# Kernel tuning notes

Measured on AMD Instinct MI355X. Metric: run time of the kernel, lower is better.

Reference implementation:

```python
import jax, jax.numpy as jnp
import numpy as np

FEAT_DIM = 128
GUIDE_DIM = 128
NIR_DIM = 32
H_LR, W_LR = 128, 128
H_HR, W_HR = 256, 256
IMNET_IN = FEAT_DIM + 2 * GUIDE_DIM + 2  # 386


def make_coord_1d(n):
    # pixel-center coords in [-1, 1]: (2i+1)/n - 1
    return (2.0 * jnp.arange(n, dtype=jnp.float32) + 1.0) / n - 1.0


def nearest_sample(img, cy, cx):
    """F.grid_sample(img, grid, mode='nearest', align_corners=False, padding='zeros').
    img: [b, C, h, w]; cy, cx: [N] normalized coords (cy -> h axis, cx -> w axis).
    Returns sampled values [b, C, N] and the pixel-center coords (qcy, qcx) the
    nearest sample corresponds to (0 when out of range, matching zero padding)."""
    h, w = img.shape[-2], img.shape[-1]
    iy = jnp.round(((cy + 1.0) * h - 1.0) * 0.5).astype(jnp.int32)  # round-half-even == nearbyint
    ix = jnp.round(((cx + 1.0) * w - 1.0) * 0.5).astype(jnp.int32)
    valid = (iy >= 0) & (iy < h) & (ix >= 0) & (ix < w)
    iyc = jnp.clip(iy, 0, h - 1)
    ixc = jnp.clip(ix, 0, w - 1)
    out = img[:, :, iyc, ixc]                       # [b, C, N] gather
    out = jnp.where(valid[None, None, :], out, 0.0)
    qcy = jnp.where(valid, (2.0 * iyc.astype(jnp.float32) + 1.0) / h - 1.0, 0.0)
    qcx = jnp.where(valid, (2.0 * ixc.astype(jnp.float32) + 1.0) / w - 1.0, 0.0)
    return out, qcy, qcx


def mlp(x, W1, b1, W2, b2, W3, b3):
    x = jax.nn.relu(x @ W1 + b1)
    x = jax.nn.relu(x @ W2 + b2)
    return x @ W3 + b3


def setup_inputs() -> dict:
    key = jax.random.key(0)
    ks = jax.random.split(key, 9)
    return {
        "feat": jax.random.normal(ks[0], (1, FEAT_DIM, H_LR, W_LR), jnp.float32),
        "lr_guide": jax.random.normal(ks[1], (1, GUIDE_DIM, H_LR, W_LR), jnp.float32),
        "hr_guide": jax.random.normal(ks[2], (1, GUIDE_DIM, H_HR, W_HR), jnp.float32),
        "W1": jax.random.normal(ks[3], (IMNET_IN, 256), jnp.float32) * 0.05,
        "b1": jax.random.normal(ks[4], (256,), jnp.float32) * 0.05,
        "W2": jax.random.normal(ks[5], (256, 128), jnp.float32) * 0.05,
        "b2": jax.random.normal(ks[6], (128,), jnp.float32) * 0.05,
        "W3": jax.random.normal(ks[7], (128, NIR_DIM), jnp.float32) * 0.05,
        "b3": jax.random.normal(ks[8], (NIR_DIM,), jnp.float32) * 0.05,
    }


def reference(feat, lr_guide, hr_guide, W1, b1, W2, b2, W3, b3):
    b, _, h, w = feat.shape
    _, cg, H, W = hr_guide.shape
    N = H * W
    featc = jnp.concatenate([lr_guide, feat], axis=1)        # [b, guide+feat, h, w]

    gy, gx = jnp.meshgrid(make_coord_1d(H), make_coord_1d(W), indexing="ij")
    cy = gy.reshape(-1)                                      # [N] coord[:, 0] (h axis)
    cx = gx.reshape(-1)                                      # [N] coord[:, 1] (w axis)

    q_guide_hr = hr_guide.reshape(b, cg, N).transpose(0, 2, 1)  # [b, N, cg]

    # feat_ : gather at the unshifted coord (identical across neighbors)
    feat_b, _, _ = nearest_sample(featc, cy, cx)
    feat_b = feat_b.transpose(0, 2, 1)                       # [b, N, C]

    rx = 1.0 / h
    ry = 1.0 / w
    preds, gcs = [], []
    for vx in (-1.0, 1.0):
        for vy in (-1.0, 1.0):
            q_feat, qcy, qcx = nearest_sample(featc, cy + vx * rx, cx + vy * ry)
            q_feat = q_feat.transpose(0, 2, 1)               # [b, N, C]
            rel = jnp.stack([(cy - qcy) * h, (cx - qcx) * w], axis=-1)  # [N, 2]
            rel = jnp.broadcast_to(rel[None], (b, N, 2))
            inp = jnp.concatenate([q_feat, q_guide_hr, rel], axis=-1)  # [b, N, 386]
            preds.append(mlp(inp, W1, b1, W2, b2, W3, b3))   # [b, N, NIR]
            # bilateral color weight: dot over channels [-4:-1]
            gcs.append(jnp.sum(feat_b[..., -4:-1] * q_feat[..., -4:-1], axis=-1))
    preds = jnp.stack(preds, axis=-1)                        # [b, N, NIR, 4]
    weight = jax.nn.softmax(jnp.stack(gcs, axis=-1), axis=-1)  # [b, N, 4]
    ret = jnp.sum(preds * weight[:, :, None, :], axis=-1)    # [b, N, NIR]
    return ret.transpose(0, 2, 1).reshape(b, -1, H, W)
```

## Files before the change

kernel.cpp:

```cpp
#include <hip/hip_runtime.h>
#include <hip/hip_bf16.h>


using bf16x8 = __attribute__((ext_vector_type(8))) __bf16;
using f32x4  = __attribute__((ext_vector_type(4))) float;

__device__ __forceinline__ float bf2f(unsigned short u){
  unsigned int x = ((unsigned int)u) << 16;
  return __builtin_bit_cast(float, x);
}
__device__ __forceinline__ unsigned short f2bf(float f){
  unsigned int x = __builtin_bit_cast(unsigned int, f);
  unsigned int r = x + 0x7fffu + ((x >> 16) & 1u);
  return (unsigned short)(r >> 16);
}
__device__ __forceinline__ bf16x8 ld8(const ushort* p){
  uint4 r = *(const uint4*)p;
  return __builtin_bit_cast(bf16x8, r);
}

struct RowMeta { int spos; float relY, relX; };
__device__ __forceinline__ RowMeta row_meta(int Y, int X, int br){
  int ivx = br >> 1, ivy = br & 1;
  int validY, iy; float relY;
  if (ivx == 0){ validY = (Y >= 1);   iy = (Y-1) >> 1; relY = (Y & 1) ?  0.5f :  1.5f; }
  else         { validY = (Y <= 254); iy = (Y+1) >> 1; relY = (Y & 1) ? -1.5f : -0.5f; }
  int validX, ix; float relX;
  if (ivy == 0){ validX = (X >= 1);   ix = (X-1) >> 1; relX = (X & 1) ?  0.5f :  1.5f; }
  else         { validX = (X <= 254); ix = (X+1) >> 1; relX = (X & 1) ? -1.5f : -0.5f; }
  RowMeta r;
  if (validY && validX){ r.spos = iy*128 + ix; r.relY = relY; r.relX = relX; }
  else { r.spos = -1; r.relY = (float)Y + 0.5f - 128.0f; r.relX = (float)X + 0.5f - 128.0f; }
  return r;
}

__global__ __launch_bounds__(256) void convert_weights(
    const float* __restrict__ W1, const float* __restrict__ W2,
    const float* __restrict__ W3,
    ushort* __restrict__ W1t,
    ushort* __restrict__ W2t,
    ushort* __restrict__ W3t)
{
  int i = blockIdx.x*256 + threadIdx.x;
  { int k = i >> 8, n = i & 255; W1t[n*384 + k] = f2bf(W1[i]); }
  if (i < 32768){ int k = i >> 7, n = i & 127; W2t[n*256 + k] = f2bf(W2[i]); }
  if (i < 4096) { int k = i >> 5, n = i & 31;  W3t[n*128 + k] = f2bf(W3[i]); }
}

__global__ __launch_bounds__(256) void stage1_gemm(
    const float* __restrict__ src0, const float* __restrict__ src1, int M,
    const ushort* __restrict__ Bt, int koff,
    const float* __restrict__ bias,
    ushort* __restrict__ outp)
{
  __shared__ ushort A[64*136];
  const int t = threadIdx.x;
  const int w = t >> 6, lane = t & 63, quad = lane >> 4, l15 = lane & 15;
  const int pos0 = blockIdx.x * 64;
  const int nhalf = src1 ? 2 : 1;

  f32x4 acc[4][4];
  #pragma unroll
  for (int mt=0; mt<4; mt++)
    #pragma unroll
    for (int nt=0; nt<4; nt++) acc[mt][nt] = f32x4{0.f,0.f,0.f,0.f};

  for (int h=0; h<nhalf; h++){
    const float* src = h ? src1 : src0;
    #pragma unroll
    for (int i=0; i<32; i++){
      int f = i*256 + t;
      int k = f >> 6, mm = f & 63;
      A[mm*136 + k] = f2bf(src[(size_t)k*M + pos0 + mm]);
    }
    __syncthreads();
    bf16x8 b[4][4];
    #pragma unroll
    for (int kt=0; kt<4; kt++)
      #pragma unroll
      for (int nt=0; nt<4; nt++)
        b[kt][nt] = ld8(&Bt[(size_t)(w*64 + nt*16 + l15)*384 + koff + h*128 + kt*32 + quad*8]);
    #pragma unroll
    for (int mt=0; mt<4; mt++)
      #pragma unroll
      for (int kt=0; kt<4; kt++){
        bf16x8 a = ld8(&A[(mt*16 + l15)*136 + kt*32 + quad*8]);
        #pragma unroll
        for (int nt=0; nt<4; nt++)
          acc[mt][nt] = __builtin_amdgcn_mfma_f32_16x16x32_bf16(a, b[kt][nt], acc[mt][nt], 0,0,0);
      }
    __syncthreads();
  }
  #pragma unroll
  for (int mt=0; mt<4; mt++)
    #pragma unroll
    for (int nt=0; nt<4; nt++){
      int n = w*64 + nt*16 + l15;
      float bv = bias ? bias[n] : 0.0f;
      #pragma unroll
      for (int r=0; r<4; r++){
        int mm = mt*16 + quad*4 + r;
        outp[(size_t)(pos0 + mm)*256 + n] = f2bf(acc[mt][nt][r] + bv);
      }
    }
}

__global__ __launch_bounds__(256, 3) void main_fused(
    const float* __restrict__ feat,
    const float* __restrict__ hr_guide,
    const float* __restrict__ W1,
    const float* __restrict__ b1v,
    const float* __restrict__ b2v,
    const float* __restrict__ b3v,
    const ushort* __restrict__ U,
    const ushort* __restrict__ W1t,
    const ushort* __restrict__ W2t,
    const ushort* __restrict__ W3t,
    float* __restrict__ outp)
{
  __shared__ __align__(16) ushort A1[64*264];
  __shared__ __align__(16) ushort Gt[16*264];
  __shared__ __align__(16) float  w1r[2][256];
  __shared__ float gcs[64];
  __shared__ float wgt[64];

  const int t = threadIdx.x;
  const int w = t >> 6, lane = t & 63, quad = lane >> 4, l15 = lane & 15;
  const int Y  = blockIdx.x >> 4;
  const int X0 = (blockIdx.x & 15) << 4;

  const int m   = t >> 2;
  const int pix = m >> 2, br = m & 3;
  const int c0  = (t & 3) * 64;
  RowMeta rm = row_meta(Y, X0 + pix, br);

  uint4 uu[8];
  if (rm.spos >= 0){
    const ushort* Up = U + (size_t)rm.spos*256 + c0;
    #pragma unroll
    for (int j=0; j<8; j++) uu[j] = *(const uint4*)(Up + j*8);
  } else {
    #pragma unroll
    for (int j=0; j<8; j++) uu[j] = make_uint4(0u,0u,0u,0u);
  }

  {
    ushort* Ahr = A1;
    #pragma unroll
    for (int i=0; i<2; i++){
      int id = i*256 + t;
      int ch = id >> 2, xq = id & 3;
      float4 v = *(const float4*)(hr_guide + (size_t)ch*65536 + Y*256 + X0 + xq*4);
      Ahr[(xq*4+0)*136 + ch] = f2bf(v.x);
      Ahr[(xq*4+1)*136 + ch] = f2bf(v.y);
      Ahr[(xq*4+2)*136 + ch] = f2bf(v.z);
      Ahr[(xq*4+3)*136 + ch] = f2bf(v.w);
    }
  }
  w1r[0][t] = W1[384*256 + t];
  w1r[1][t] = W1[385*256 + t];

  if (t < 64){
    RowMeta g = row_meta(Y, X0 + (t>>2), t & 3);
    float gc = 0.0f;
    if (g.spos >= 0){
      int bpos = (Y>>1)*128 + ((X0 + (t>>2)) >> 1);
      #pragma unroll
      for (int cc=0; cc<3; cc++)
        gc += feat[(size_t)(124+cc)*16384 + bpos] * feat[(size_t)(124+cc)*16384 + g.spos];
    }
    gcs[t] = gc;
  }
  __syncthreads();

  if (t < 16){
    float g0 = gcs[t*4+0], g1 = gcs[t*4+1], g2 = gcs[t*4+2], g3 = gcs[t*4+3];
    float mx = fmaxf(fmaxf(g0,g1), fmaxf(g2,g3));
    float e0 = __expf(g0-mx), e1 = __expf(g1-mx), e2 = __expf(g2-mx), e3 = __expf(g3-mx);
    float inv = 1.0f/(e0+e1+e2+e3);
    wgt[t*4+0]=e0*inv; wgt[t*4+1]=e1*inv; wgt[t*4+2]=e2*inv; wgt[t*4+3]=e3*inv;
  }
  {
    f32x4 accg[4];
    #pragma unroll
    for (int nt=0; nt<4; nt++) accg[nt] = f32x4{0.f,0.f,0.f,0.f};
    #pragma unroll
    for (int kt=0; kt<4; kt++){
      bf16x8 a = ld8(&A1[l15*136 + kt*32 + quad*8]);
      #pragma unroll
      for (int nt=0; nt<4; nt++){
        bf16x8 b = ld8(&W1t[(size_t)(w*64 + nt*16 + l15)*384 + 256 + kt*32 + quad*8]);
        accg[nt] = __builtin_amdgcn_mfma_f32_16x16x32_bf16(a, b, accg[nt], 0,0,0);
      }
    }
    #pragma unroll
    for (int nt=0; nt<4; nt++){
      int n = w*64 + nt*16 + l15;
      float bv = b1v[n];
      #pragma unroll
      for (int r=0; r<4; r++)
        Gt[(quad*4+r)*264 + n] = f2bf(accg[nt][r] + bv);
    }
  }
  __syncthreads();

  bf16x8 b2f[8][2];
  #pragma unroll
  for (int kt=0; kt<8; kt++)
    #pragma unroll
    for (int nt=0; nt<2; nt++)
      b2f[kt][nt] = ld8(&W2t[(size_t)(w*32 + nt*16 + l15)*256 + kt*32 + quad*8]);

  {
    float relY = rm.relY, relX = rm.relX;
    #pragma unroll
    for (int jj=0; jj<8; jj++){
      int c = c0 + jj*8;
      union { uint4 v; ushort s[8]; } gu, uv, ov;
      gu.v = *(const uint4*)&Gt[pix*264 + c];
      uv.v = uu[jj];
      float r0[8], r1[8];
      *(float4*)&r0[0] = *(const float4*)&w1r[0][c];
      *(float4*)&r0[4] = *(const float4*)&w1r[0][c+4];
      *(float4*)&r1[0] = *(const float4*)&w1r[1][c];
      *(float4*)&r1[4] = *(const float4*)&w1r[1][c+4];
      #pragma unroll
      for (int i=0; i<8; i++){
        float h = bf2f(uv.s[i]) + bf2f(gu.s[i]) + relY*r0[i] + relX*r1[i];
        ov.s[i] = f2bf(fmaxf(h, 0.0f));
      }
      *(uint4*)&A1[m*264 + c] = ov.v;
    }
  }
  __syncthreads();

  f32x4 acc2[4][2];
  #pragma unroll
  for (int mt=0; mt<4; mt++)
    #pragma unroll
    for (int nt=0; nt<2; nt++) acc2[mt][nt] = f32x4{0.f,0.f,0.f,0.f};
  #pragma unroll
  for (int mt=0; mt<4; mt++)
    #pragma unroll
    for (int kt=0; kt<8; kt++){
      bf16x8 a = ld8(&A1[(mt*16 + l15)*264 + kt*32 + quad*8]);
      #pragma unroll
      for (int nt=0; nt<2; nt++)
        acc2[mt][nt] = __builtin_amdgcn_mfma_f32_16x16x32_bf16(a, b2f[kt][nt], acc2[mt][nt], 0,0,0);
    }
  __syncthreads();

  bf16x8 b3f[4][2];
  #pragma unroll
  for (int kt=0; kt<4; kt++)
    #pragma unroll
    for (int nt=0; nt<2; nt++)
      b3f[kt][nt] = ld8(&W3t[(size_t)(nt*16 + l15)*128 + kt*32 + quad*8]);

  {
    ushort* A2 = A1;
    float bias0 = b2v[w*32 + l15], bias1 = b2v[w*32 + 16 + l15];
    #pragma unroll
    for (int mt=0; mt<4; mt++)
      #pragma unroll
      for (int nt=0; nt<2; nt++){
        int n = w*32 + nt*16 + l15;
        float bv = nt ? bias1 : bias0;
        #pragma unroll
        for (int r=0; r<4; r++){
          int mm = mt*16 + quad*4 + r;
          A2[mm*136 + n] = f2bf(fmaxf(acc2[mt][nt][r] + bv, 0.0f));
        }
      }
  }
  __syncthreads();

  {
    const ushort* A2 = A1;
    f32x4 acc3[2] = { f32x4{0.f,0.f,0.f,0.f}, f32x4{0.f,0.f,0.f,0.f} };
    #pragma unroll
    for (int kt=0; kt<4; kt++){
      bf16x8 a = ld8(&A2[(w*16 + l15)*136 + kt*32 + quad*8]);
      #pragma unroll
      for (int nt=0; nt<2; nt++)
        acc3[nt] = __builtin_amdgcn_mfma_f32_16x16x32_bf16(a, b3f[kt][nt], acc3[nt], 0,0,0);
    }
    int lp = w*4 + quad;
    int X = X0 + lp;
    float w0 = wgt[lp*4+0], w1 = wgt[lp*4+1], w2 = wgt[lp*4+2], w3 = wgt[lp*4+3];
    #pragma unroll
    for (int nt=0; nt<2; nt++){
      int n = nt*16 + l15;
      float bb = b3v[n];
      float v = w0*(acc3[nt][0]+bb) + w1*(acc3[nt][1]+bb)
              + w2*(acc3[nt][2]+bb) + w3*(acc3[nt][3]+bb);
      outp[(size_t)n*65536 + (size_t)Y*256 + X] = v;
    }
  }
}

extern "C" void kernel_launch(void* const* d_in, const int* in_sizes, int n_in,
                              void* d_out, int out_size, void* d_ws, size_t ws_size,
                              hipStream_t stream)
{
  const float* feat     = (const float*)d_in[0];
  const float* lr_guide = (const float*)d_in[1];
  const float* hr_guide = (const float*)d_in[2];
  const float* W1       = (const float*)d_in[3];
  const float* b1       = (const float*)d_in[4];
  const float* W2       = (const float*)d_in[5];
  const float* b2       = (const float*)d_in[6];
  const float* W3       = (const float*)d_in[7];
  const float* b3       = (const float*)d_in[8];
  float* outp = (float*)d_out;

  char* ws = (char*)d_ws;
  ushort* W1t = (ushort*)(ws);
  ushort* W2t = (ushort*)(ws + 196608);
  ushort* W3t = (ushort*)(ws + 196608 + 65536);
  ushort* Ub  = (ushort*)(ws + 196608 + 65536 + 8192);

  convert_weights<<<384, 256, 0, stream>>>(W1, W2, W3, W1t, W2t, W3t);
  stage1_gemm<<<256, 256, 0, stream>>>(lr_guide, feat, 16384, W1t, 0, nullptr, Ub);
  main_fused<<<4096, 256, 0, stream>>>(feat, hr_guide, W1, b1, b2, b3,
                                       Ub, W1t, W2t, W3t, outp);
}
```

Measured before the change: 204.1 us.

## Fold layer-1 gather, rel and bias terms into a single MFMA K-slice

The layer-1 epilogue used to gather precomputed U rows, add the hr-guide GEMM result and apply the rel/bias terms in scalar code. It now appends a fifth MFMA K-step whose A operand holds gathered U entries plus the rel weights and bias rows, and whose B operand is a one-hot selector built per row. That removes the Gt staging buffer, one barrier and the scalar pass, and lets occupancy rise to 4 blocks. The stage-1 GEMM is also split into smaller 32-row, half-N blocks so more of them launch. The cost is scattered 2-byte gathers from Ub and some extra MFMA work.

After: 207.8 us. Within noise of the previous version (+1.8%).

```diff
diff --git a/kernel.cpp b/kernel.cpp
--- a/kernel.cpp
+++ b/kernel.cpp
@@ -19,7 +19,7 @@
   return __builtin_bit_cast(bf16x8, r);
 }
 
-struct RowMeta { int spos; float relY, relX; };
+struct RowMeta { int valid, ix; float relY, relX; int spos; };
 __device__ __forceinline__ RowMeta row_meta(int Y, int X, int br){
   int ivx = br >> 1, ivy = br & 1;
   int validY, iy; float relY;
@@ -29,98 +29,96 @@
   if (ivy == 0){ validX = (X >= 1);   ix = (X-1) >> 1; relX = (X & 1) ?  0.5f :  1.5f; }
   else         { validX = (X <= 254); ix = (X+1) >> 1; relX = (X & 1) ? -1.5f : -0.5f; }
   RowMeta r;
-  if (validY && validX){ r.spos = iy*128 + ix; r.relY = relY; r.relX = relX; }
-  else { r.spos = -1; r.relY = (float)Y + 0.5f - 128.0f; r.relX = (float)X + 0.5f - 128.0f; }
+  r.valid = validY && validX;
+  r.ix = ix;
+  if (r.valid){ r.relY = relY; r.relX = relX; r.spos = iy*128 + ix; }
+  else { r.relY = (float)Y + 0.5f - 128.0f; r.relX = (float)X + 0.5f - 128.0f; r.spos = -1; }
   return r;
 }
 
 __global__ __launch_bounds__(256) void convert_weights(
-    const float* __restrict__ W1, const float* __restrict__ W2,
-    const float* __restrict__ W3,
+    const float* __restrict__ W1, const float* __restrict__ b1,
+    const float* __restrict__ W2, const float* __restrict__ W3,
     ushort* __restrict__ W1t,
     ushort* __restrict__ W2t,
-    ushort* __restrict__ W3t)
+    ushort* __restrict__ W3t,
+    ushort* __restrict__ Ub)
 {
-  int i = blockIdx.x*256 + threadIdx.x;
-  { int k = i >> 8, n = i & 255; W1t[n*384 + k] = f2bf(W1[i]); }
-  if (i < 32768){ int k = i >> 7, n = i & 127; W2t[n*256 + k] = f2bf(W2[i]); }
-  if (i < 4096) { int k = i >> 5, n = i & 31;  W3t[n*128 + k] = f2bf(W3[i]); }
+  int b = blockIdx.x, t = threadIdx.x;
+  if (b < 384){
+    int i = b*256 + t;
+    { int k = i >> 8, n = i & 255; W1t[n*384 + k] = f2bf(W1[i]); }
+    if (i < 32768){ int k = i >> 7, n = i & 127; W2t[n*256 + k] = f2bf(W2[i]); }
+    if (i < 4096) { int k = i >> 5, n = i & 31;  W3t[n*128 + k] = f2bf(W3[i]); }
+  } else {
+    int r = b - 384;
+    float v = (r == 0) ? W1[384*256 + t] : (r == 1) ? W1[385*256 + t]
+            : (r == 2) ? b1[t] : 0.0f;
+    Ub[(size_t)(16384 + r)*256 + t] = f2bf(v);
+  }
 }
 
 __global__ __launch_bounds__(256) void stage1_gemm(
-    const float* __restrict__ src0, const float* __restrict__ src1, int M,
-    const ushort* __restrict__ Bt, int koff,
-    const float* __restrict__ bias,
+    const float* __restrict__ src0, const float* __restrict__ src1,
+    const ushort* __restrict__ W1t,
     ushort* __restrict__ outp)
 {
-  __shared__ ushort A[64*136];
+  __shared__ ushort A[32*136];
   const int t = threadIdx.x;
   const int w = t >> 6, lane = t & 63, quad = lane >> 4, l15 = lane & 15;
-  const int pos0 = blockIdx.x * 64;
-  const int nhalf = src1 ? 2 : 1;
-
-  f32x4 acc[4][4];
-  #pragma unroll
-  for (int mt=0; mt<4; mt++)
-    #pragma unroll
-    for (int nt=0; nt<4; nt++) acc[mt][nt] = f32x4{0.f,0.f,0.f,0.f};
-
-  for (int h=0; h<nhalf; h++){
+  const int pos0  = (blockIdx.x >> 1) * 32;
+  const int nside = (blockIdx.x & 1) * 128;
+  const int mt = w >> 1;
+  const int ntb = (w & 1) * 4;
+
+  f32x4 acc[4];
+  #pragma unroll
+  for (int nt=0; nt<4; nt++) acc[nt] = f32x4{0.f,0.f,0.f,0.f};
+
+  for (int h=0; h<2; h++){
     const float* src = h ? src1 : src0;
     #pragma unroll
-    for (int i=0; i<32; i++){
+    for (int i=0; i<16; i++){
       int f = i*256 + t;
-      int k = f >> 6, mm = f & 63;
-      A[mm*136 + k] = f2bf(src[(size_t)k*M + pos0 + mm]);
+      int k = f >> 5, mm = f & 31;
+      A[mm*136 + k] = f2bf(src[(size_t)k*16384 + pos0 + mm]);
     }
     __syncthreads();
-    bf16x8 b[4][4];
-    #pragma unroll
-    for (int kt=0; kt<4; kt++)
-      #pragma unroll
-      for (int nt=0; nt<4; nt++)
-        b[kt][nt] = ld8(&Bt[(size_t)(w*64 + nt*16 + l15)*384 + koff + h*128 + kt*32 + quad*8]);
-    #pragma unroll
-    for (int mt=0; mt<4; mt++)
-      #pragma unroll
-      for (int kt=0; kt<4; kt++){
-        bf16x8 a = ld8(&A[(mt*16 + l15)*136 + kt*32 + quad*8]);
-        #pragma unroll
-        for (int nt=0; nt<4; nt++)
-          acc[mt][nt] = __builtin_amdgcn_mfma_f32_16x16x32_bf16(a, b[kt][nt], acc[mt][nt], 0,0,0);
+    #pragma unroll
+    for (int kt=0; kt<4; kt++){
+      bf16x8 a = ld8(&A[(mt*16 + l15)*136 + kt*32 + quad*8]);
+      #pragma unroll
+      for (int nt=0; nt<4; nt++){
+        bf16x8 b = ld8(&W1t[(size_t)(nside + (ntb+nt)*16 + l15)*384 + h*128 + kt*32 + quad*8]);
+        acc[nt] = __builtin_amdgcn_mfma_f32_16x16x32_bf16(a, b, acc[nt], 0,0,0);
       }
+    }
     __syncthreads();
   }
   #pragma unroll
-  for (int mt=0; mt<4; mt++)
-    #pragma unroll
-    for (int nt=0; nt<4; nt++){
-      int n = w*64 + nt*16 + l15;
-      float bv = bias ? bias[n] : 0.0f;
-      #pragma unroll
-      for (int r=0; r<4; r++){
-        int mm = mt*16 + quad*4 + r;
-        outp[(size_t)(pos0 + mm)*256 + n] = f2bf(acc[mt][nt][r] + bv);
-      }
-    }
-}
-
-__global__ __launch_bounds__(256, 3) void main_fused(
+  for (int nt=0; nt<4; nt++){
+    int n = nside + (ntb+nt)*16 + l15;
+    #pragma unroll
+    for (int r=0; r<4; r++){
+      int mm = mt*16 + quad*4 + r;
+      outp[(size_t)(pos0 + mm)*256 + n] = f2bf(acc[nt][r]);
+    }
+  }
+}
+
+__global__ __launch_bounds__(256, 4) void main_fused(
     const float* __restrict__ feat,
     const float* __restrict__ hr_guide,
-    const float* __restrict__ W1,
-    const float* __restrict__ b1v,
     const float* __restrict__ b2v,
     const float* __restrict__ b3v,
-    const ushort* __restrict__ U,
+    const ushort* __restrict__ Ub,
     const ushort* __restrict__ W1t,
     const ushort* __restrict__ W2t,
     const ushort* __restrict__ W3t,
     float* __restrict__ outp)
 {
   __shared__ __align__(16) ushort A1[64*264];
-  __shared__ __align__(16) ushort Gt[16*264];
-  __shared__ __align__(16) float  w1r[2][256];
+  __shared__ __align__(16) ushort Ahr[16*136];
   __shared__ float gcs[64];
   __shared__ float wgt[64];
 
@@ -128,38 +126,19 @@
   const int w = t >> 6, lane = t & 63, quad = lane >> 4, l15 = lane & 15;
   const int Y  = blockIdx.x >> 4;
   const int X0 = (blockIdx.x & 15) << 4;
-
-  const int m   = t >> 2;
-  const int pix = m >> 2, br = m & 3;
-  const int c0  = (t & 3) * 64;
-  RowMeta rm = row_meta(Y, X0 + pix, br);
-
-  uint4 uu[8];
-  if (rm.spos >= 0){
-    const ushort* Up = U + (size_t)rm.spos*256 + c0;
-    #pragma unroll
-    for (int j=0; j<8; j++) uu[j] = *(const uint4*)(Up + j*8);
-  } else {
-    #pragma unroll
-    for (int j=0; j<8; j++) uu[j] = make_uint4(0u,0u,0u,0u);
-  }
-
-  {
-    ushort* Ahr = A1;
-    #pragma unroll
-    for (int i=0; i<2; i++){
-      int id = i*256 + t;
-      int ch = id >> 2, xq = id & 3;
-      float4 v = *(const float4*)(hr_guide + (size_t)ch*65536 + Y*256 + X0 + xq*4);
-      Ahr[(xq*4+0)*136 + ch] = f2bf(v.x);
-      Ahr[(xq*4+1)*136 + ch] = f2bf(v.y);
-      Ahr[(xq*4+2)*136 + ch] = f2bf(v.z);
-      Ahr[(xq*4+3)*136 + ch] = f2bf(v.w);
-    }
-  }
-  w1r[0][t] = W1[384*256 + t];
-  w1r[1][t] = W1[385*256 + t];
-
+  const int iyA = (Y-1) >> 1, iyB = (Y+1) >> 1;
+  const int ixbase = (X0-1) >> 1;
+
+  #pragma unroll
+  for (int i=0; i<2; i++){
+    int id = i*256 + t;
+    int ch = id >> 2, xq = id & 3;
+    float4 v = *(const float4*)(hr_guide + (size_t)ch*65536 + Y*256 + X0 + xq*4);
+    Ahr[(xq*4+0)*136 + ch] = f2bf(v.x);
+    Ahr[(xq*4+1)*136 + ch] = f2bf(v.y);
+    Ahr[(xq*4+2)*136 + ch] = f2bf(v.z);
+    Ahr[(xq*4+3)*136 + ch] = f2bf(v.w);
+  }
   if (t < 64){
     RowMeta g = row_meta(Y, X0 + (t>>2), t & 3);
     float gc = 0.0f;
@@ -172,7 +151,6 @@
     gcs[t] = gc;
   }
   __syncthreads();
-
   if (t < 16){
     float g0 = gcs[t*4+0], g1 = gcs[t*4+1], g2 = gcs[t*4+2], g3 = gcs[t*4+3];
     float mx = fmaxf(fmaxf(g0,g1), fmaxf(g2,g3));
@@ -180,26 +158,66 @@
     float inv = 1.0f/(e0+e1+e2+e3);
     wgt[t*4+0]=e0*inv; wgt[t*4+1]=e1*inv; wgt[t*4+2]=e2*inv; wgt[t*4+3]=e3*inv;
   }
-  {
-    f32x4 accg[4];
-    #pragma unroll
-    for (int nt=0; nt<4; nt++) accg[nt] = f32x4{0.f,0.f,0.f,0.f};
-    #pragma unroll
-    for (int kt=0; kt<4; kt++){
-      bf16x8 a = ld8(&A1[l15*136 + kt*32 + quad*8]);
-      #pragma unroll
-      for (int nt=0; nt<4; nt++){
-        bf16x8 b = ld8(&W1t[(size_t)(w*64 + nt*16 + l15)*384 + 256 + kt*32 + quad*8]);
-        accg[nt] = __builtin_amdgcn_mfma_f32_16x16x32_bf16(a, b, accg[nt], 0,0,0);
-      }
-    }
-    #pragma unroll
-    for (int nt=0; nt<4; nt++){
-      int n = w*64 + nt*16 + l15;
-      float bv = b1v[n];
-      #pragma unroll
-      for (int r=0; r<4; r++)
-        Gt[(quad*4+r)*264 + n] = f2bf(accg[nt][r] + bv);
+
+  int uoff[8];
+  #pragma unroll
+  for (int j=0; j<8; j++){
+    int s = quad*8 + j;
+    int u = s - 3;
+    int iy = (u < 10) ? iyA : iyB;
+    int ix = ixbase + (u - ((u < 10) ? 0 : 10));
+    iy = min(max(iy, 0), 127); ix = min(max(ix, 0), 127);
+    int rid = iy*128 + ix;
+    rid = (s == 0) ? 16384 : (s == 1) ? 16385 : (s == 2) ? 16386
+        : (s >= 23) ? 16387 : rid;
+    uoff[j] = rid * 256;
+  }
+  bf16x8 bk4[4];
+  #pragma unroll
+  for (int ct=0; ct<4; ct++){
+    int m = 16*ct + l15;
+    int pix = m >> 2, br = m & 3;
+    RowMeta rm = row_meta(Y, X0 + pix, br);
+    int sstar = rm.valid ? ((br >> 1)*10 + (rm.ix - ixbase) + 3) : -1;
+    union { bf16x8 v; ushort s[8]; } bb;
+    #pragma unroll
+    for (int j=0; j<8; j++){
+      int s = quad*8 + j;
+      unsigned short val = 0;
+      if (s == 0) val = f2bf(rm.relY);
+      else if (s == 1) val = f2bf(rm.relX);
+      else if (s == 2) val = 0x3F80u;
+      if (s == sstar) val = 0x3F80u;
+      bb.s[j] = val;
+    }
+    bk4[ct] = bb.v;
+  }
+  #pragma unroll
+  for (int i=0; i<4; i++){
+    int n = w*64 + i*16 + l15;
+    const ushort* wp = W1t + (size_t)n*384 + 256;
+    bf16x8 a0 = ld8(wp + 0*32 + quad*8);
+    bf16x8 a1 = ld8(wp + 1*32 + quad*8);
+    bf16x8 a2 = ld8(wp + 2*32 + quad*8);
+    bf16x8 a3 = ld8(wp + 3*32 + quad*8);
+    union { bf16x8 v; ushort s[8]; } a4;
+    #pragma unroll
+    for (int j=0; j<8; j++) a4.s[j] = Ub[(size_t)(uoff[j] + n)];
+    #pragma unroll
+    for (int ct=0; ct<4; ct++){
+      const ushort* hp = &Ahr[(4*ct + (l15>>2))*136 + quad*8];
+      f32x4 acc = f32x4{0.f,0.f,0.f,0.f};
+      acc = __builtin_amdgcn_mfma_f32_16x16x32_bf16(a0, ld8(hp +  0), acc, 0,0,0);
+      acc = __builtin_amdgcn_mfma_f32_16x16x32_bf16(a1, ld8(hp + 32), acc, 0,0,0);
+      acc = __builtin_amdgcn_mfma_f32_16x16x32_bf16(a2, ld8(hp + 64), acc, 0,0,0);
+      acc = __builtin_amdgcn_mfma_f32_16x16x32_bf16(a3, ld8(hp + 96), acc, 0,0,0);
+      acc = __builtin_amdgcn_mfma_f32_16x16x32_bf16(a4.v, bk4[ct], acc, 0,0,0);
+      int mrow = 16*ct + l15;
+      int n0 = w*64 + i*16 + quad*4;
+      uint2 o;
+      o.x = (unsigned)f2bf(fmaxf(acc[0],0.f)) | ((unsigned)f2bf(fmaxf(acc[1],0.f)) << 16);
+      o.y = (unsigned)f2bf(fmaxf(acc[2],0.f)) | ((unsigned)f2bf(fmaxf(acc[3],0.f)) << 16);
+      *(uint2*)&A1[mrow*264 + n0] = o;
     }
   }
   __syncthreads();
@@ -211,29 +229,6 @@
     for (int nt=0; nt<2; nt++)
       b2f[kt][nt] = ld8(&W2t[(size_t)(w*32 + nt*16 + l15)*256 + kt*32 + quad*8]);
 
-  {
-    float relY = rm.relY, relX = rm.relX;
-    #pragma unroll
-    for (int jj=0; jj<8; jj++){
-      int c = c0 + jj*8;
-      union { uint4 v; ushort s[8]; } gu, uv, ov;
-      gu.v = *(const uint4*)&Gt[pix*264 + c];
-      uv.v = uu[jj];
-      float r0[8], r1[8];
-      *(float4*)&r0[0] = *(const float4*)&w1r[0][c];
-      *(float4*)&r0[4] = *(const float4*)&w1r[0][c+4];
-      *(float4*)&r1[0] = *(const float4*)&w1r[1][c];
-      *(float4*)&r1[4] = *(const float4*)&w1r[1][c+4];
-      #pragma unroll
-      for (int i=0; i<8; i++){
-        float h = bf2f(uv.s[i]) + bf2f(gu.s[i]) + relY*r0[i] + relX*r1[i];
-        ov.s[i] = f2bf(fmaxf(h, 0.0f));
-      }
-      *(uint4*)&A1[m*264 + c] = ov.v;
-    }
-  }
-  __syncthreads();
-
   f32x4 acc2[4][2];
   #pragma unroll
   for (int mt=0; mt<4; mt++)
@@ -249,13 +244,6 @@
         acc2[mt][nt] = __builtin_amdgcn_mfma_f32_16x16x32_bf16(a, b2f[kt][nt], acc2[mt][nt], 0,0,0);
     }
   __syncthreads();
-
-  bf16x8 b3f[4][2];
-  #pragma unroll
-  for (int kt=0; kt<4; kt++)
-    #pragma unroll
-    for (int nt=0; nt<2; nt++)
-      b3f[kt][nt] = ld8(&W3t[(size_t)(nt*16 + l15)*128 + kt*32 + quad*8]);
 
   {
     ushort* A2 = A1;
@@ -276,6 +264,13 @@
   __syncthreads();
 
   {
+    bf16x8 b3f[4][2];
+    #pragma unroll
+    for (int kt=0; kt<4; kt++)
+      #pragma unroll
+      for (int nt=0; nt<2; nt++)
+        b3f[kt][nt] = ld8(&W3t[(size_t)(nt*16 + l15)*128 + kt*32 + quad*8]);
+
     const ushort* A2 = A1;
     f32x4 acc3[2] = { f32x4{0.f,0.f,0.f,0.f}, f32x4{0.f,0.f,0.f,0.f} };
     #pragma unroll
@@ -320,8 +315,8 @@
   ushort* W3t = (ushort*)(ws + 196608 + 65536);
   ushort* Ub  = (ushort*)(ws + 196608 + 65536 + 8192);
 
-  convert_weights<<<384, 256, 0, stream>>>(W1, W2, W3, W1t, W2t, W3t);
-  stage1_gemm<<<256, 256, 0, stream>>>(lr_guide, feat, 16384, W1t, 0, nullptr, Ub);
-  main_fused<<<4096, 256, 0, stream>>>(feat, hr_guide, W1, b1, b2, b3,
+  convert_weights<<<388, 256, 0, stream>>>(W1, b1, W2, W3, W1t, W2t, W3t, Ub);
+  stage1_gemm<<<1024, 256, 0, stream>>>(lr_guide, feat, W1t, Ub);
+  main_fused<<<4096, 256, 0, stream>>>(feat, hr_guide, b2, b3,
                                        Ub, W1t, W2t, W3t, outp);
 }
```
